# Performance work log

Hardware: AMD Instinct MI355X
Metric: run time of the kernel (lower is better)

The kernel has to match this reference:

```python
import jax, jax.numpy as jnp
import numpy as np

B, IN, OUT, NW = 8192, 4096, 4096, 16
NH, ND2 = NW // 3, NW // 3          # 5 haar, 5 db2
ND4 = NW - NH - ND2                  # 6 db4

DB2_HI = jnp.array([-0.1294095225512604, -0.2241438680420134,
                    0.8365163037378079, -0.4829629131445341], dtype=jnp.float32)
DB4_HI = jnp.array([-0.0074578275060427, -0.0233534968567756, 0.0218081502370024,
                    0.1323683939878645, -0.0197721859913265, -0.4461007108737368,
                    0.5055922216746659, -0.1629171572809054], dtype=jnp.float32)


def setup_inputs() -> dict:
    key = jax.random.key(0)
    ks = jax.random.split(key, 4)
    x = jax.random.normal(ks[0], (B, IN), dtype=jnp.float32)
    # kaiming-normal fan_in linear init -> std = 1/sqrt(fan_in); biases zero
    lin_w = jax.random.normal(ks[1], (OUT, IN), dtype=jnp.float32) * (1.0 / np.sqrt(IN))
    lin_b = jnp.zeros((OUT,), jnp.float32)
    proj_w = jax.random.normal(ks[2], (NW, IN), dtype=jnp.float32) * (1.0 / np.sqrt(IN))
    proj_b = jnp.zeros((NW,), jnp.float32)
    # exact _init_parameters values for the 'mixed' case
    scales = jnp.concatenate([jnp.logspace(-0.5, 0.5, NH),
                              jnp.logspace(-0.3, 0.7, ND2),
                              jnp.logspace(-0.3, 0.7, ND4)]).astype(jnp.float32)
    translations = jnp.concatenate([jnp.linspace(-1.5, 1.5, NH),
                                    jnp.linspace(-1.5, 1.5, ND2),
                                    jnp.linspace(-1.5, 1.5, ND4)]).astype(jnp.float32)
    comb_w = jax.random.normal(ks[3], (OUT, NW), dtype=jnp.float32) * (1.0 / np.sqrt(NW))
    comb_b = jnp.zeros((OUT,), jnp.float32)
    ln_g = jnp.ones((OUT,), jnp.float32)
    ln_beta = jnp.zeros((OUT,), jnp.float32)
    return dict(x=x, lin_w=lin_w, lin_b=lin_b, proj_w=proj_w, proj_b=proj_b,
                scales=scales, translations=translations,
                comb_w=comb_w, comb_b=comb_b, ln_g=ln_g, ln_beta=ln_beta)


def _haar_mother(sx):
    # Haar mother wavelet: +1 on [0, 0.5), -1 on [0.5, 1)
    return (((sx >= 0.0) & (sx < 0.5)).astype(jnp.float32)
            - ((sx >= 0.5) & (sx < 1.0)).astype(jnp.float32))


def _db_feature(val, scale, trans, filt, max_shift, mult):
    # db*_wavelet_transform + simplified_transform (scalar per wavelet)
    scale_factor = jax.nn.sigmoid(scale) * 2.0
    shift = jnp.clip(jnp.round(trans * mult), 0, max_shift).astype(jnp.int32)
    f = jnp.roll(filt, shift) * scale_factor
    feat = jnp.mean(val * jnp.sin(f * 5.0))
    return feat / (jnp.sum(jnp.abs(f)) * 0.1)  # filter_sum always > 0 here


def reference(x, lin_w, lin_b, proj_w, proj_b, scales, translations,
              comb_w, comb_b, ln_g, ln_beta):
    direct = x @ lin_w.T + lin_b                 # [B, OUT]
    proj = x @ proj_w.T + proj_b                 # [B, NW]

    # Haar wavelets on first NH projected channels (elementwise, per batch)
    sx = (proj[:, :NH] - translations[:NH]) / scales[:NH]
    haar = _haar_mother(sx)                      # [B, NH]

    # Daubechies 'simplified_transform': mean of first min(4,B) batch entries per column
    vals = jnp.mean(proj[:4, :], axis=0)         # [NW]
    db2 = jax.vmap(lambda v, s, t: _db_feature(v, s, t, DB2_HI, 3, 4.0))(
        vals[NH:NH + ND2], scales[NH:NH + ND2], translations[NH:NH + ND2])
    db4 = jax.vmap(lambda v, s, t: _db_feature(v, s, t, DB4_HI, 7, 8.0))(
        vals[NH + ND2:], scales[NH + ND2:], translations[NH + ND2:])
    db = jnp.broadcast_to(jnp.concatenate([db2, db4])[None, :],
                          (x.shape[0], ND2 + ND4))  # [B, ND2+ND4]

    wave = jnp.concatenate([haar, db], axis=1)   # [B, NW]
    wave_path = wave @ comb_w.T + comb_b         # [B, OUT]

    y = direct + wave_path
    mu = jnp.mean(y, axis=-1, keepdims=True)
    var = jnp.mean((y - mu) ** 2, axis=-1, keepdims=True)
    return (y - mu) * jax.lax.rsqrt(var + 1e-5) * ln_g + ln_beta
```

## Files before the change

### kernel.cpp

```cpp
#include <hip/hip_runtime.h>
#include <hip/hip_bf16.h>
#include <stdint.h>

constexpr int BDIM = 8192;
constexpr int INDIM = 4096;
constexpr int OUTDIM = 4096;

typedef __attribute__((ext_vector_type(8))) short bf16x8;
typedef __attribute__((ext_vector_type(8))) short short8;
typedef __attribute__((ext_vector_type(4))) float f32x4;

__device__ __forceinline__ uint16_t f2bf_rne(float f) {
  union { float f; uint32_t u; } v; v.f = f;
  uint32_t r = v.u + 0x7fffu + ((v.u >> 16) & 1u);
  return (uint16_t)(r >> 16);
}
__device__ __forceinline__ float bf2f(uint16_t h) {
  union { uint32_t u; float f; } v; v.u = ((uint32_t)h) << 16; return v.f;
}

__device__ __forceinline__ void gload_lds16(const void* g, void* l) {
  __builtin_amdgcn_global_load_lds(
      (const __attribute__((address_space(1))) void*)g,
      (__attribute__((address_space(3))) void*)l, 16, 0, 0);
}

__global__ __launch_bounds__(256) void k_pre(
    const float* __restrict__ x, const float* __restrict__ lin_w,
    const float* __restrict__ proj_w, const float* __restrict__ proj_b,
    const float* __restrict__ scales, const float* __restrict__ trans,
    const float* __restrict__ lin_b, const float* __restrict__ comb_w,
    const float* __restrict__ comb_b, uint16_t* __restrict__ xb,
    uint16_t* __restrict__ wb, float* __restrict__ haar,
    float* __restrict__ cvec, float* __restrict__ W5) {
  __shared__ float sh[96];
  const int tid = threadIdx.x;
  const int lane = tid & 63, w = tid >> 6;

  if (blockIdx.x < 2048) {
    const int row0 = blockIdx.x * 4;
    const float4* xr0 = (const float4*)(x + (size_t)(row0 + 0) * INDIM);
    const float4* xr1 = (const float4*)(x + (size_t)(row0 + 1) * INDIM);
    const float4* xr2 = (const float4*)(x + (size_t)(row0 + 2) * INDIM);
    const float4* xr3 = (const float4*)(x + (size_t)(row0 + 3) * INDIM);
    ushort4* xb0 = (ushort4*)(xb + (size_t)(row0 + 0) * INDIM);
    ushort4* xb1 = (ushort4*)(xb + (size_t)(row0 + 1) * INDIM);
    ushort4* xb2 = (ushort4*)(xb + (size_t)(row0 + 2) * INDIM);
    ushort4* xb3 = (ushort4*)(xb + (size_t)(row0 + 3) * INDIM);
    const float4* pw4 = (const float4*)proj_w;
    float acc[4][5];
#pragma unroll
    for (int r = 0; r < 4; ++r)
#pragma unroll
      for (int j = 0; j < 5; ++j) acc[r][j] = 0.f;

#pragma unroll
    for (int c = 0; c < 4; ++c) {
      const int i4 = tid + c * 256;
      float4 p[5];
#pragma unroll
      for (int j = 0; j < 5; ++j) p[j] = pw4[j * 1024 + i4];
      const float4* xr[4] = {xr0, xr1, xr2, xr3};
      ushort4* xo[4] = {xb0, xb1, xb2, xb3};
#pragma unroll
      for (int r = 0; r < 4; ++r) {
        float4 v = xr[r][i4];
        ushort4 o;
        o.x = f2bf_rne(v.x); o.y = f2bf_rne(v.y);
        o.z = f2bf_rne(v.z); o.w = f2bf_rne(v.w);
        xo[r][i4] = o;
#pragma unroll
        for (int j = 0; j < 5; ++j)
          acc[r][j] += v.x * p[j].x + v.y * p[j].y + v.z * p[j].z + v.w * p[j].w;
      }
    }
#pragma unroll
    for (int r = 0; r < 4; ++r)
#pragma unroll
      for (int j = 0; j < 5; ++j) {
        float v = acc[r][j];
#pragma unroll
        for (int off = 32; off; off >>= 1) v += __shfl_down(v, off, 64);
        if (lane == 0) sh[(w * 4 + r) * 5 + j] = v;
      }
    __syncthreads();
    if (tid < 20) {
      const int r = tid / 5, j = tid % 5;
      float pv = sh[(0 * 4 + r) * 5 + j] + sh[(1 * 4 + r) * 5 + j] +
                 sh[(2 * 4 + r) * 5 + j] + sh[(3 * 4 + r) * 5 + j] + proj_b[j];
      float sx = (pv - trans[j]) / scales[j];
      float h = 0.f;
      if (sx >= 0.f && sx < 0.5f) h = 1.f;
      else if (sx >= 0.5f && sx < 1.f) h = -1.f;
      haar[(size_t)(row0 + r) * 5 + j] = h;
    }
  } else if (blockIdx.x < 4096) {
    const int bid = blockIdx.x - 2048;
    const int n8 = (OUTDIM * INDIM) / 8;
    const float4* w4 = (const float4*)lin_w;
    short8* wb8 = (short8*)wb;
    for (int i = bid * 256 + tid; i < n8; i += 2048 * 256) {
      float4 v0 = w4[i * 2];
      float4 v1 = w4[i * 2 + 1];
      short8 o;
      o[0] = (short)f2bf_rne(v0.x); o[1] = (short)f2bf_rne(v0.y);
      o[2] = (short)f2bf_rne(v0.z); o[3] = (short)f2bf_rne(v0.w);
      o[4] = (short)f2bf_rne(v1.x); o[5] = (short)f2bf_rne(v1.y);
      o[6] = (short)f2bf_rne(v1.z); o[7] = (short)f2bf_rne(v1.w);
      wb8[i] = o;
    }
  } else {
    float* wred = sh;
    float* dbs = sh + 64;
    float acc[11];
#pragma unroll
    for (int j = 0; j < 11; ++j) acc[j] = 0.f;
    for (int r = 0; r < 4; ++r) {
      const float4* xr = (const float4*)(x + (size_t)r * INDIM);
      for (int c = tid; c < INDIM / 4; c += 256) {
        float4 v = xr[c];
#pragma unroll
        for (int j = 0; j < 11; ++j) {
          float4 p = ((const float4*)(proj_w + (size_t)(j + 5) * INDIM))[c];
          acc[j] += v.x * p.x + v.y * p.y + v.z * p.z + v.w * p.w;
        }
      }
    }
#pragma unroll
    for (int j = 0; j < 11; ++j) {
      float v = acc[j];
#pragma unroll
      for (int off = 32; off; off >>= 1) v += __shfl_down(v, off, 64);
      if (lane == 0) wred[w * 11 + j] = v;
    }
    __syncthreads();
    if (tid == 0) {
      const float DB2[4] = {-0.1294095225512604f, -0.2241438680420134f,
                            0.8365163037378079f, -0.4829629131445341f};
      const float DB4[8] = {-0.0074578275060427f, -0.0233534968567756f,
                            0.0218081502370024f,  0.1323683939878645f,
                            -0.0197721859913265f, -0.4461007108737368f,
                            0.5055922216746659f,  -0.1629171572809054f};
      for (int j = 0; j < 11; ++j) {
        float sum = wred[0 * 11 + j] + wred[1 * 11 + j] + wred[2 * 11 + j] +
                    wred[3 * 11 + j];
        float val = sum * 0.25f + proj_b[j + 5];
        float sc = scales[j + 5];
        float sf = 2.f / (1.f + expf(-sc));
        const float* filt = (j < 5) ? DB2 : DB4;
        int L = (j < 5) ? 4 : 8;
        float ssin = 0.f, sabs = 0.f;
        for (int i = 0; i < L; ++i) {
          float fi = filt[i] * sf;
          ssin += sinf(fi * 5.0f);
          sabs += fabsf(fi);
        }
        dbs[j] = val * (ssin / (float)L) / (sabs * 0.1f);
      }
    }
    __syncthreads();
    for (int o = tid; o < OUTDIM; o += 256) {
      const float* cw = comb_w + (size_t)o * 16;
      float cc = lin_b[o] + comb_b[o];
#pragma unroll
      for (int j = 0; j < 11; ++j) cc += dbs[j] * cw[5 + j];
      cvec[o] = cc;
#pragma unroll
      for (int j = 0; j < 5; ++j) W5[j * OUTDIM + o] = cw[j];
    }
  }
}


#define BARX() __builtin_amdgcn_s_barrier()
#define LGKM0() do { asm volatile("s_waitcnt lgkmcnt(0)" ::: "memory"); \
                     __builtin_amdgcn_sched_barrier(0); } while (0)
#define VM6() asm volatile("s_waitcnt vmcnt(6)" ::: "memory")

#define STAGE_A(t, q) do { \
  const char* _s = aSrc + (size_t)(q) * 64 * 8192 + (size_t)((t) & 63) * 128; \
  char* _l = sA + ((t) & 1) * 32768 + (q) * 8192 + ldsStage; \
  gload_lds16(_s, _l); gload_lds16(_s + 128 * 8192, _l + 16384); } while (0)

#define STAGE_B(t, h) do { \
  const char* _s = bSrc + (size_t)(h) * 128 * 8192 + (size_t)((t) & 63) * 128; \
  char* _l = sB + ((t) & 1) * 32768 + (h) * 16384 + ldsStage; \
  gload_lds16(_s, _l); gload_lds16(_s + 64 * 8192, _l + 8192); } while (0)

#define RDA4(buf, mb) do { const char* _p = sA + (buf) * 32768; \
  _Pragma("unroll") for (int _m = 0; _m < 4; ++_m) { \
    ar[_m][0] = *(const bf16x8*)(_p + (aoff + ((mb) + _m) * 2048)); \
    ar[_m][1] = *(const bf16x8*)(_p + ((aoff ^ 64) + ((mb) + _m) * 2048)); } } while (0)

#define RDB2(buf, arr, nb) do { const char* _p = sB + (buf) * 32768; \
  _Pragma("unroll") for (int _n = 0; _n < 2; ++_n) { \
    arr[_n][0] = *(const bf16x8*)(_p + (boff + ((nb) + _n) * 2048)); \
    arr[_n][1] = *(const bf16x8*)(_p + ((boff ^ 64) + ((nb) + _n) * 2048)); } } while (0)

#define MF8(mb, arrB, nb) do { \
  __builtin_amdgcn_s_setprio(1); \
  _Pragma("unroll") for (int _m = 0; _m < 4; ++_m) \
  _Pragma("unroll") for (int _n = 0; _n < 2; ++_n) { \
    acc[(mb) + _m][(nb) + _n] = __builtin_amdgcn_mfma_f32_16x16x32_bf16( \
        ar[_m][0], arrB[_n][0], acc[(mb) + _m][(nb) + _n], 0, 0, 0); \
    acc[(mb) + _m][(nb) + _n] = __builtin_amdgcn_mfma_f32_16x16x32_bf16( \
        ar[_m][1], arrB[_n][1], acc[(mb) + _m][(nb) + _n], 0, 0, 0); } \
  __builtin_amdgcn_s_setprio(0); } while (0)

template <bool WB>
__global__ __launch_bounds__(512, 2) void k_gemm(const uint16_t* __restrict__ A,
                                                 const uint16_t* __restrict__ Bw,
                                                 float* __restrict__ C,
                                                 uint16_t* __restrict__ Ybf) {
  constexpr int K = INDIM;
  constexpr int N = OUTDIM;
  extern __shared__ char smem[];
  char* sA = smem;
  char* sB = smem + 65536;

  const int tid = threadIdx.x;
  const int wid = tid >> 6;
  const int lane = tid & 63;
  const int l15 = lane & 15;
  const int kh = lane >> 4;
  const int wm = wid >> 2;
  const int wn = wid & 3;

  const int nwg = gridDim.x;
  const int bid = blockIdx.x;
  const int wg = (bid & 7) * (nwg >> 3) + (bid >> 3);
  constexpr int NBN = N / 256;
  const int mblk = wg / NBN, nblk = wg % NBN;
  const size_t arow = (size_t)mblk * 256, brow = (size_t)nblk * 256;

  const int srow = tid >> 3;
  const int scol = ((tid & 7) * 16) ^ ((srow & 7) << 4);
  const char* aSrc = (const char*)A + (arow + srow) * 8192 + scol;
  const char* bSrc = (const char*)Bw + (brow + srow) * 8192 + scol;
  const int ldsStage = wid * 1024;

  const int col0 = (kh * 16) ^ ((l15 & 7) << 4);
  const int aoff = (wm * 128 + l15) * 128 + col0;
  const int boff = (wn * 64 + l15) * 128 + col0;

  f32x4 acc[8][4];
#pragma unroll
  for (int m = 0; m < 8; ++m)
#pragma unroll
    for (int n = 0; n < 4; ++n) acc[m][n] = (f32x4){0.f, 0.f, 0.f, 0.f};
  bf16x8 ar[4][2], b01[2][2], b23[2][2];

  STAGE_A(0, 0); STAGE_A(0, 1); STAGE_B(0, 0); STAGE_B(0, 1);
  STAGE_A(1, 0); STAGE_B(1, 0); STAGE_B(1, 1);
  VM6(); BARX();

  for (int it = 0; it < K / 128; ++it) {
    const int t1 = it * 2 + 1, t2 = it * 2 + 2, t3 = it * 2 + 3;
    RDA4(0, 0); RDB2(0, b01, 0);
    STAGE_A(t1, 1);
    LGKM0(); BARX(); MF8(0, b01, 0);
    RDB2(0, b23, 2);
    STAGE_A(t2, 0);
    LGKM0(); BARX(); MF8(0, b23, 2);
    RDA4(0, 4);
    STAGE_B(t2, 0);
    LGKM0(); BARX(); MF8(4, b01, 0);
    STAGE_B(t2, 1);
    LGKM0(); VM6(); BARX(); MF8(4, b23, 2);
    RDA4(1, 0); RDB2(1, b01, 0);
    STAGE_A(t2, 1);
    LGKM0(); BARX(); MF8(0, b01, 0);
    RDB2(1, b23, 2);
    STAGE_A(t3, 0);
    LGKM0(); BARX(); MF8(0, b23, 2);
    RDA4(1, 4);
    STAGE_B(t3, 0);
    LGKM0(); BARX(); MF8(4, b01, 0);
    STAGE_B(t3, 1);
    LGKM0(); VM6(); BARX(); MF8(4, b23, 2);
  }

  const size_t crow0 = arow + (size_t)wm * 128;
  const int ccol0 = (int)brow + wn * 64;
#pragma unroll
  for (int m = 0; m < 8; ++m) {
#pragma unroll
    for (int n = 0; n < 4; ++n) {
      if constexpr (WB) {
        uint16_t* yp = Ybf + (crow0 + m * 16 + kh * 4) * (size_t)N
                       + ccol0 + n * 16 + l15;
#pragma unroll
        for (int j = 0; j < 4; ++j) yp[(size_t)j * N] = f2bf_rne(acc[m][n][j]);
      } else {
        float* cp = C + (crow0 + m * 16 + kh * 4) * N + ccol0 + n * 16 + l15;
#pragma unroll
        for (int j = 0; j < 4; ++j) cp[(size_t)j * N] = acc[m][n][j];
      }
    }
  }
}

template <bool RB>
__global__ __launch_bounds__(256) void k_ln(
    float* __restrict__ out, const uint16_t* __restrict__ ybf,
    const float* __restrict__ haar, const float* __restrict__ cvec,
    const float* __restrict__ W5, const float* __restrict__ g,
    const float* __restrict__ beta) {
  const int tid = threadIdx.x, lane = tid & 63, w = tid >> 6;
  const int row0 = blockIdx.x * 4;
  float h[4][5];
#pragma unroll
  for (int r = 0; r < 4; ++r)
#pragma unroll
    for (int j = 0; j < 5; ++j) h[r][j] = haar[(size_t)(row0 + r) * 5 + j];

  const ushort4* yb[4];
  const float4* yf[4];
  float4* yo[4];
#pragma unroll
  for (int r = 0; r < 4; ++r) {
    yb[r] = (const ushort4*)(ybf + (size_t)(row0 + r) * OUTDIM);
    yf[r] = (const float4*)(out + (size_t)(row0 + r) * OUTDIM);
    yo[r] = (float4*)(out + (size_t)(row0 + r) * OUTDIM);
  }

  float4 vals[4][4];
  float s[4] = {0.f, 0.f, 0.f, 0.f}, s2[4] = {0.f, 0.f, 0.f, 0.f};
#pragma unroll
  for (int c = 0; c < 4; ++c) {
    const int i4 = tid + c * 256;
    float4 cv = ((const float4*)cvec)[i4];
    float4 w0 = ((const float4*)(W5 + 0 * OUTDIM))[i4];
    float4 w1 = ((const float4*)(W5 + 1 * OUTDIM))[i4];
    float4 w2 = ((const float4*)(W5 + 2 * OUTDIM))[i4];
    float4 w3 = ((const float4*)(W5 + 3 * OUTDIM))[i4];
    float4 w4 = ((const float4*)(W5 + 4 * OUTDIM))[i4];
#pragma unroll
    for (int r = 0; r < 4; ++r) {
      float4 d;
      if constexpr (RB) {
        ushort4 u = yb[r][i4];
        d.x = bf2f(u.x); d.y = bf2f(u.y); d.z = bf2f(u.z); d.w = bf2f(u.w);
      } else {
        d = yf[r][i4];
      }
      float4 t;
      t.x = d.x + cv.x + h[r][0]*w0.x + h[r][1]*w1.x + h[r][2]*w2.x + h[r][3]*w3.x + h[r][4]*w4.x;
      t.y = d.y + cv.y + h[r][0]*w0.y + h[r][1]*w1.y + h[r][2]*w2.y + h[r][3]*w3.y + h[r][4]*w4.y;
      t.z = d.z + cv.z + h[r][0]*w0.z + h[r][1]*w1.z + h[r][2]*w2.z + h[r][3]*w3.z + h[r][4]*w4.z;
      t.w = d.w + cv.w + h[r][0]*w0.w + h[r][1]*w1.w + h[r][2]*w2.w + h[r][3]*w3.w + h[r][4]*w4.w;
      vals[r][c] = t;
      s[r] += t.x + t.y + t.z + t.w;
      s2[r] += t.x * t.x + t.y * t.y + t.z * t.z + t.w * t.w;
    }
  }

  __shared__ float rs[4][4], rs2[4][4];
#pragma unroll
  for (int r = 0; r < 4; ++r) {
    float a = s[r], b = s2[r];
#pragma unroll
    for (int off = 32; off; off >>= 1) {
      a += __shfl_down(a, off, 64);
      b += __shfl_down(b, off, 64);
    }
    if (lane == 0) { rs[w][r] = a; rs2[w][r] = b; }
  }
  __syncthreads();
  float mu[4], inv[4];
#pragma unroll
  for (int r = 0; r < 4; ++r) {
    float S = rs[0][r] + rs[1][r] + rs[2][r] + rs[3][r];
    float S2 = rs2[0][r] + rs2[1][r] + rs2[2][r] + rs2[3][r];
    mu[r] = S / (float)OUTDIM;
    inv[r] = rsqrtf(S2 / (float)OUTDIM - mu[r] * mu[r] + 1e-5f);
  }
#pragma unroll
  for (int c = 0; c < 4; ++c) {
    const int i4 = tid + c * 256;
    float4 gg = ((const float4*)g)[i4];
    float4 bb = ((const float4*)beta)[i4];
#pragma unroll
    for (int r = 0; r < 4; ++r) {
      float4 t = vals[r][c];
      float4 o;
      o.x = (t.x - mu[r]) * inv[r] * gg.x + bb.x;
      o.y = (t.y - mu[r]) * inv[r] * gg.y + bb.y;
      o.z = (t.z - mu[r]) * inv[r] * gg.z + bb.z;
      o.w = (t.w - mu[r]) * inv[r] * gg.w + bb.w;
      yo[r][i4] = o;
    }
  }
}

extern "C" void kernel_launch(void* const* d_in, const int* in_sizes, int n_in,
                              void* d_out, int out_size, void* d_ws, size_t ws_size,
                              hipStream_t stream) {
  const float* x      = (const float*)d_in[0];
  const float* lin_w  = (const float*)d_in[1];
  const float* lin_b  = (const float*)d_in[2];
  const float* proj_w = (const float*)d_in[3];
  const float* proj_b = (const float*)d_in[4];
  const float* scales = (const float*)d_in[5];
  const float* trans  = (const float*)d_in[6];
  const float* comb_w = (const float*)d_in[7];
  const float* comb_b = (const float*)d_in[8];
  const float* ln_g   = (const float*)d_in[9];
  const float* ln_b   = (const float*)d_in[10];
  float* out = (float*)d_out;

  char* ws = (char*)d_ws;
  uint16_t* xb   = (uint16_t*)ws;
  uint16_t* wb   = (uint16_t*)(ws + 67108864);
  float*    haar = (float*)(ws + 100663296);
  float*    cvec = (float*)(ws + 100827136);
  float*    W5   = (float*)(ws + 100843520);
  uint16_t* ybf  = (uint16_t*)(ws + 100925440);
  const bool bf16y = ws_size >= 168034304ull;

  hipFuncSetAttribute((const void*)k_gemm<true>,
                      hipFuncAttributeMaxDynamicSharedMemorySize, 131072);
  hipFuncSetAttribute((const void*)k_gemm<false>,
                      hipFuncAttributeMaxDynamicSharedMemorySize, 131072);

  k_pre<<<4097, 256, 0, stream>>>(x, lin_w, proj_w, proj_b, scales, trans,
                                  lin_b, comb_w, comb_b, xb, wb, haar, cvec, W5);
  if (bf16y) {
    k_gemm<true><<<(BDIM / 256) * (OUTDIM / 256), 512, 131072, stream>>>(
        xb, wb, out, ybf);
    k_ln<true><<<BDIM / 4, 256, 0, stream>>>(out, ybf, haar, cvec, W5, ln_g, ln_b);
  } else {
    k_gemm<false><<<(BDIM / 256) * (OUTDIM / 256), 512, 131072, stream>>>(
        xb, wb, out, ybf);
    k_ln<false><<<BDIM / 4, 256, 0, stream>>>(out, ybf, haar, cvec, W5, ln_g, ln_b);
  }
}
```

Baseline: 338.5 us.

## Double-buffer A fragment registers and use partial lgkmcnt waits in GEMM loop

Splits the A register fragment into two sets so the second half of the A tile is read from LDS while the first MFMA group runs. LDS reads are issued earlier and waited on with partial lgkmcnt counts instead of full drains. The global-to-LDS staging order is reshuffled, with one B stage moved into an earlier slot and the vmcnt threshold lowered. The goal is to hide LDS read latency behind MFMA work. The cost is extra VGPRs under a 512x2 launch bound, plus a risk of wrong counts or LDS buffer races given the changed stage order.

```diff
diff --git a/kernel.cpp b/kernel.cpp
--- a/kernel.cpp
+++ b/kernel.cpp
@@ -172,10 +172,11 @@
 }
 
 
-#define BARX() __builtin_amdgcn_s_barrier()
-#define LGKM0() do { asm volatile("s_waitcnt lgkmcnt(0)" ::: "memory"); \
-                     __builtin_amdgcn_sched_barrier(0); } while (0)
-#define VM6() asm volatile("s_waitcnt vmcnt(6)" ::: "memory")
+#define SB0() __builtin_amdgcn_sched_barrier(0)
+#define BARX() do { __builtin_amdgcn_s_barrier(); SB0(); } while (0)
+#define LGKM(n) do { asm volatile("s_waitcnt lgkmcnt(" #n ")" ::: "memory"); \
+                     SB0(); } while (0)
+#define VMC(n) asm volatile("s_waitcnt vmcnt(" #n ")" ::: "memory")
 
 #define STAGE_A(t, q) do { \
   const char* _s = aSrc + (size_t)(q) * 64 * 8192 + (size_t)((t) & 63) * 128; \
@@ -187,24 +188,24 @@
   char* _l = sB + ((t) & 1) * 32768 + (h) * 16384 + ldsStage; \
   gload_lds16(_s, _l); gload_lds16(_s + 64 * 8192, _l + 8192); } while (0)
 
-#define RDA4(buf, mb) do { const char* _p = sA + (buf) * 32768; \
+#define RDA4(arr, buf, mb) do { const char* _p = sA + (buf) * 32768; \
   _Pragma("unroll") for (int _m = 0; _m < 4; ++_m) { \
-    ar[_m][0] = *(const bf16x8*)(_p + (aoff + ((mb) + _m) * 2048)); \
-    ar[_m][1] = *(const bf16x8*)(_p + ((aoff ^ 64) + ((mb) + _m) * 2048)); } } while (0)
+    arr[_m][0] = *(const bf16x8*)(_p + (aoff + ((mb) + _m) * 2048)); \
+    arr[_m][1] = *(const bf16x8*)(_p + ((aoff ^ 64) + ((mb) + _m) * 2048)); } } while (0)
 
 #define RDB2(buf, arr, nb) do { const char* _p = sB + (buf) * 32768; \
   _Pragma("unroll") for (int _n = 0; _n < 2; ++_n) { \
     arr[_n][0] = *(const bf16x8*)(_p + (boff + ((nb) + _n) * 2048)); \
     arr[_n][1] = *(const bf16x8*)(_p + ((boff ^ 64) + ((nb) + _n) * 2048)); } } while (0)
 
-#define MF8(mb, arrB, nb) do { \
+#define MF8(arrA, mb, arrB, nb) do { \
   __builtin_amdgcn_s_setprio(1); \
   _Pragma("unroll") for (int _m = 0; _m < 4; ++_m) \
   _Pragma("unroll") for (int _n = 0; _n < 2; ++_n) { \
     acc[(mb) + _m][(nb) + _n] = __builtin_amdgcn_mfma_f32_16x16x32_bf16( \
-        ar[_m][0], arrB[_n][0], acc[(mb) + _m][(nb) + _n], 0, 0, 0); \
+        arrA[_m][0], arrB[_n][0], acc[(mb) + _m][(nb) + _n], 0, 0, 0); \
     acc[(mb) + _m][(nb) + _n] = __builtin_amdgcn_mfma_f32_16x16x32_bf16( \
-        ar[_m][1], arrB[_n][1], acc[(mb) + _m][(nb) + _n], 0, 0, 0); } \
+        arrA[_m][1], arrB[_n][1], acc[(mb) + _m][(nb) + _n], 0, 0, 0); } \
   __builtin_amdgcn_s_setprio(0); } while (0)
 
 template <bool WB>
@@ -248,36 +249,38 @@
   for (int m = 0; m < 8; ++m)
 #pragma unroll
     for (int n = 0; n < 4; ++n) acc[m][n] = (f32x4){0.f, 0.f, 0.f, 0.f};
-  bf16x8 ar[4][2], b01[2][2], b23[2][2];
+  bf16x8 ar[4][2], ar2[4][2], b01[2][2], b23[2][2];
 
   STAGE_A(0, 0); STAGE_A(0, 1); STAGE_B(0, 0); STAGE_B(0, 1);
-  STAGE_A(1, 0); STAGE_B(1, 0); STAGE_B(1, 1);
-  VM6(); BARX();
+  STAGE_A(1, 0); STAGE_B(1, 0);
+  VMC(4); BARX();
 
   for (int it = 0; it < K / 128; ++it) {
     const int t1 = it * 2 + 1, t2 = it * 2 + 2, t3 = it * 2 + 3;
-    RDA4(0, 0); RDB2(0, b01, 0);
+    RDA4(ar, 0, 0); RDB2(0, b01, 0);
+    SB0();
+    RDB2(0, b23, 2);
     STAGE_A(t1, 1);
-    LGKM0(); BARX(); MF8(0, b01, 0);
-    RDB2(0, b23, 2);
+    LGKM(4); BARX(); MF8(ar, 0, b01, 0);
+    RDA4(ar2, 0, 4);
+    STAGE_B(t1, 1);
+    LGKM(8); BARX(); MF8(ar, 0, b23, 2);
     STAGE_A(t2, 0);
-    LGKM0(); BARX(); MF8(0, b23, 2);
-    RDA4(0, 4);
+    LGKM(0); BARX(); MF8(ar2, 4, b01, 0);
     STAGE_B(t2, 0);
-    LGKM0(); BARX(); MF8(4, b01, 0);
+    VMC(4); BARX(); MF8(ar2, 4, b23, 2);
+    RDA4(ar, 1, 0); RDB2(1, b01, 0);
+    SB0();
+    RDB2(1, b23, 2);
+    STAGE_A(t2, 1);
+    LGKM(4); BARX(); MF8(ar, 0, b01, 0);
+    RDA4(ar2, 1, 4);
     STAGE_B(t2, 1);
-    LGKM0(); VM6(); BARX(); MF8(4, b23, 2);
-    RDA4(1, 0); RDB2(1, b01, 0);
-    STAGE_A(t2, 1);
-    LGKM0(); BARX(); MF8(0, b01, 0);
-    RDB2(1, b23, 2);
+    LGKM(8); BARX(); MF8(ar, 0, b23, 2);
     STAGE_A(t3, 0);
-    LGKM0(); BARX(); MF8(0, b23, 2);
-    RDA4(1, 4);
+    LGKM(0); BARX(); MF8(ar2, 4, b01, 0);
     STAGE_B(t3, 0);
-    LGKM0(); BARX(); MF8(4, b01, 0);
-    STAGE_B(t3, 1);
-    LGKM0(); VM6(); BARX(); MF8(4, b23, 2);
+    VMC(4); BARX(); MF8(ar2, 4, b23, 2);
   }
 
   const size_t crow0 = arow + (size_t)wm * 128;
```

After: 381.4 us. +12.7%, slower.
